# Kernel optimization log

Hardware: AMD Instinct MI355X
Metric: run time of the kernel (lower is better)

The kernel has to match this reference:

```python
import jax, jax.numpy as jnp
import numpy as np

B, L = 1024, 64          # sentences, tokens per sentence
V, E = 100000, 300       # vocab, embedding dim
RH, M, NC = 50, 50, 3    # rnn_hidden, mem_dim, num_class
N = B * L                # total tree nodes


def setup_inputs() -> dict:
    key = jax.random.key(0)
    ks = jax.random.split(key, 24)
    rn = lambda k, s, sc=0.05: jax.random.normal(k, s, dtype=jnp.float32) * sc
    # balanced binary dependency tree per sentence: parent(i) = (i-1)//2
    loc = np.arange(L)
    par_loc = np.where(loc == 0, -1, (loc - 1) // 2)
    parent = np.where(par_loc[None, :] < 0, -1,
                      par_loc[None, :] + np.arange(B)[:, None] * L).reshape(-1)
    depth = np.tile(np.floor(np.log2(loc + 1)).astype(np.int64), B)
    tm = np.zeros(L, np.float32); tm[1:4] = 1.0  # 3 aspect-target tokens/sentence
    return {
        "embed_ids": jax.random.randint(ks[0], (B, L), 0, V),
        "parent": jnp.asarray(parent),
        "depth": jnp.asarray(depth),
        "target_mask": jnp.asarray(np.tile(tm, B)),
        "num_levels": 7,
        "embed_table": rn(ks[1], (V, E), 1.0),
        "W_ih_f": rn(ks[2], (4 * RH, E)), "W_hh_f": rn(ks[3], (4 * RH, RH)),
        "b_f": rn(ks[4], (4 * RH,)),
        "W_ih_b": rn(ks[5], (4 * RH, E)), "W_hh_b": rn(ks[6], (4 * RH, RH)),
        "b_b": rn(ks[7], (4 * RH,)),
        "W_iou": rn(ks[8], (3 * M, 2 * RH)),
        "U_iou_w": rn(ks[9], (3 * M, M)), "U_iou_b": rn(ks[10], (3 * M,)),
        "b_iou": jnp.zeros((3 * M,), jnp.float32),
        "U_f_w": rn(ks[11], (M, M)), "U_f_b": rn(ks[12], (M,)),
        "H_w": rn(ks[13], (M, 2 * RH)), "H_b": rn(ks[14], (M,)),
        "C_w": rn(ks[15], (NC, M)), "C_b": rn(ks[16], (NC,)),
    }


def _lstm(x, W_ih, W_hh, b, reverse):
    # x: (B, L, E) -> (B, L, H); PyTorch gate order i, f, g, o
    xg = jnp.einsum('ble,ge->blg', x, W_ih) + b
    H = W_hh.shape[1]
    def step(carry, xt):
        h, c = carry
        g = xt + h @ W_hh.T
        i, f, gg, o = jnp.split(g, 4, axis=-1)
        c = jax.nn.sigmoid(f) * c + jax.nn.sigmoid(i) * jnp.tanh(gg)
        h = jax.nn.sigmoid(o) * jnp.tanh(c)
        return (h, c), h
    z = jnp.zeros((x.shape[0], H), x.dtype)
    _, hs = jax.lax.scan(step, (z, z), jnp.swapaxes(xg, 0, 1), reverse=reverse)
    return jnp.swapaxes(hs, 0, 1)


def reference(embed_ids, parent, depth, target_mask, num_levels, embed_table,
              W_ih_f, W_hh_f, b_f, W_ih_b, W_hh_b, b_b,
              W_iou, U_iou_w, U_iou_b, b_iou, U_f_w, U_f_b,
              H_w, H_b, C_w, C_b):
    # --- BiLSTM encoder (dropout = identity at inference) ---
    emb = embed_table[embed_ids]                       # (B,L,E) gather
    hf = _lstm(emb, W_ih_f, W_hh_f, b_f, False)
    hb = _lstm(emb, W_ih_b, W_hh_b, b_b, True)
    x = jnp.concatenate([hf, hb], -1).reshape(N, 2 * RH)
    # --- ChildSum TreeLSTM, topological (deepest level first) ---
    iou0 = x @ W_iou.T                                 # (N, 3M)
    h_init = x @ H_w.T + H_b                           # (N, M)
    parent_safe = jnp.where(parent >= 0, parent, N)    # roots -> dummy slot N
    counts = jnp.zeros(N + 1, jnp.int32).at[parent_safe].add(1)
    has_children = (counts[:N] > 0)[:, None]
    h_fin = h_init
    c_fin = jnp.zeros((N, M), jnp.float32)
    h_sum = jnp.zeros((N + 1, M), jnp.float32)         # sum of child h
    fc_sum = jnp.zeros((N + 1, M), jnp.float32)        # sum of f * child c
    for lvl in range(num_levels - 1, -1, -1):
        m = (depth == lvl)[:, None]
        # reduce: leaves never get U_iou bias (no mailbox in DGL)
        iou = iou0 + jnp.where(has_children, h_sum[:N] @ U_iou_w.T + U_iou_b, 0.0) + b_iou
        i, o, u = jnp.split(iou, 3, axis=-1)
        c_new = jax.nn.sigmoid(i) * jnp.tanh(u) + fc_sum[:N]
        h_new = h_init + jax.nn.sigmoid(o) * jnp.tanh(c_new)
        h_fin = jnp.where(m, h_new, h_fin)
        c_fin = jnp.where(m, c_new, c_fin)
        # scatter messages from this level's nodes to their parents
        f = jax.nn.sigmoid(h_new @ U_f_w.T + U_f_b)
        h_sum = h_sum.at[parent_safe].add(jnp.where(m, h_new, 0.0))
        fc_sum = fc_sum.at[parent_safe].add(jnp.where(m, f * c_new, 0.0))
    # --- masked mean pool over target tokens per sentence ---
    tm = target_mask.reshape(B, L)
    pooled = (h_fin.reshape(B, L, M) * tm[:, :, None]).sum(1) / tm.sum(1, keepdims=True)
    logits = pooled @ C_w.T + C_b
    return logits, pooled
```

## Files before the change

kernel.cpp:

```cpp
#include <hip/hip_runtime.h>


typedef __attribute__((ext_vector_type(8))) short bf16x8;
typedef __attribute__((ext_vector_type(4))) float f32x4;

__device__ __forceinline__ float fsig2(float x) {
    float e = __builtin_amdgcn_exp2f(-1.4426950408889634f * x);
    return __builtin_amdgcn_rcpf(1.0f + e);
}
__device__ __forceinline__ float ftanh2(float x) {
    float e = __builtin_amdgcn_exp2f(2.8853900817779268f * x);
    return 1.0f - 2.0f * __builtin_amdgcn_rcpf(1.0f + e);
}

__device__ __forceinline__ unsigned short rne_bf16(float f) {
    unsigned u = __builtin_bit_cast(unsigned, f);
    unsigned r = u + 0x7fffu + ((u >> 16) & 1u);
    return (unsigned short)(r >> 16);
}
__device__ __forceinline__ void split2(float f, unsigned short& h, unsigned short& l) {
    h = rne_bf16(f);
    float fh = __builtin_bit_cast(float, ((unsigned)h) << 16);
    float r = f - fh;
    l = rne_bf16(r);
}

__device__ __forceinline__ void async_lds16(const void* g, void* l) {
    __builtin_amdgcn_global_load_lds(
        (const __attribute__((address_space(1))) unsigned int*)g,
        (__attribute__((address_space(3))) unsigned int*)l, 16, 0, 0);
}

__device__ __forceinline__ bf16x8 pack8(const unsigned short* h) {
    bf16x8 v;
    #pragma unroll
    for (int e = 0; e < 8; ++e) v[e] = (short)h[e];
    return v;
}

__device__ __forceinline__ void conv_item(int q, const float* __restrict__ B1,
                                          const float* __restrict__ B2,
                                          int split, int K, int Rreal, int BN,
                                          unsigned short* __restrict__ out) {
    int n  = q % BN;
    int kq = (q / BN) & 3;
    int c  = q / (BN * 4);
    const float* row = (n < split) ? (B1 + (size_t)n * K) : (B2 + (size_t)(n - split) * K);
    unsigned short h[8], l[8];
    #pragma unroll
    for (int e = 0; e < 8; ++e) {
        int k = c * 32 + kq * 8 + e;
        float v = (n < Rreal && k < K) ? row[k] : 0.0f;
        split2(v, h[e], l[e]);
    }
    size_t hb = ((((size_t)c * 2 + 0) * 4 + kq) * BN + n) * 8;
    size_t lb = ((((size_t)c * 2 + 1) * 4 + kq) * BN + n) * 8;
    *(ushort4*)&out[hb]     = make_ushort4(h[0], h[1], h[2], h[3]);
    *(ushort4*)&out[hb + 4] = make_ushort4(h[4], h[5], h[6], h[7]);
    *(ushort4*)&out[lb]     = make_ushort4(l[0], l[1], l[2], l[3]);
    *(ushort4*)&out[lb + 4] = make_ushort4(l[4], l[5], l[6], l[7]);
}

constexpr int WHC_DIR = 2 * 2 * 4 * 208 * 8;

__global__ void conv_fused(const float* __restrict__ Wihf, const float* __restrict__ Wihb,
                           const float* __restrict__ Wiou, const float* __restrict__ Hw,
                           const float* __restrict__ Whhf, const float* __restrict__ Whhb,
                           unsigned short* __restrict__ B1c,
                           unsigned short* __restrict__ B3c,
                           unsigned short* __restrict__ Whc) {
    int q = blockIdx.x * 256 + threadIdx.x;
    if (q < 17920) {
        conv_item(q, Wihf, Wihb, 200, 300, 400, 448, B1c);
    } else if (q < 22016) {
        conv_item(q - 17920, Wiou, Hw, 150, 100, 200, 256, B3c);
    } else if (q < 23680) {
        conv_item(q - 22016, Whhf, Whhf, 200, 50, 200, 208, Whc);
    } else if (q < 25344) {
        conv_item(q - 23680, Whhb, Whhb, 200, 50, 200, 208, Whc + WHC_DIR);
    }
}

template<int BN, int KCH, int KREAL, int NCOLS, bool GATHER>
__global__ __launch_bounds__(256)
void gemm_split(const float* __restrict__ A, const int* __restrict__ ids,
                const unsigned short* __restrict__ Bc,
                const float* __restrict__ bias1, const float* __restrict__ bias2,
                int split, float* __restrict__ C) {
    constexpr int NTW = BN / 64;
    __shared__ __align__(16) unsigned short As[2 * 4 * 64 * 8];
    __shared__ __align__(16) unsigned short Bt[64 * BN];

    const int tid = threadIdx.x;
    const int m0 = blockIdx.x * 64;
    const int w = tid >> 6, lane = tid & 63;
    const int r16 = lane & 15, quad = lane >> 4;
    const int wn = w * (BN / 4);

    const int mA = tid & 63, kqA = tid >> 6;
    const float* arow = GATHER ? (A + (size_t)ids[m0 + mA] * KREAL)
                               : (A + (size_t)(m0 + mA) * KREAL);

    float ar[8];
    {
        int k0 = kqA * 8;
        if (k0 + 8 <= KREAL) {
            float4 p = *(const float4*)(arow + k0);
            float4 q = *(const float4*)(arow + k0 + 4);
            ar[0]=p.x; ar[1]=p.y; ar[2]=p.z; ar[3]=p.w;
            ar[4]=q.x; ar[5]=q.y; ar[6]=q.z; ar[7]=q.w;
        } else {
            #pragma unroll
            for (int e = 0; e < 8; ++e) ar[e] = (k0 + e < KREAL) ? arow[k0 + e] : 0.0f;
        }
    }

    f32x4 acc[4][NTW] = {};

    for (int c = 0; c < KCH; ++c) {
        __syncthreads();
        {
            const unsigned short* src = Bc + (size_t)c * 64 * BN + tid * 8;
            #pragma unroll
            for (int i = 0; i < BN / 32; ++i)
                async_lds16(src + (size_t)i * 2048, Bt + i * 2048 + tid * 8);
        }
        {
            unsigned short h[8], l[8];
            #pragma unroll
            for (int e = 0; e < 8; ++e) split2(ar[e], h[e], l[e]);
            *(bf16x8*)&As[((0 * 4 + kqA) * 64 + mA) * 8] = pack8(h);
            *(bf16x8*)&As[((1 * 4 + kqA) * 64 + mA) * 8] = pack8(l);
        }
        __syncthreads();
        if (c + 1 < KCH) {
            int k0 = (c + 1) * 32 + kqA * 8;
            if (k0 + 8 <= KREAL) {
                float4 p = *(const float4*)(arow + k0);
                float4 q = *(const float4*)(arow + k0 + 4);
                ar[0]=p.x; ar[1]=p.y; ar[2]=p.z; ar[3]=p.w;
                ar[4]=q.x; ar[5]=q.y; ar[6]=q.z; ar[7]=q.w;
            } else {
                #pragma unroll
                for (int e = 0; e < 8; ++e) ar[e] = (k0 + e < KREAL) ? arow[k0 + e] : 0.0f;
            }
        }
        bf16x8 af[2][4];
        #pragma unroll
        for (int i = 0; i < 4; ++i) {
            af[0][i] = *(const bf16x8*)&As[((0 * 4 + quad) * 64 + i * 16 + r16) * 8];
            af[1][i] = *(const bf16x8*)&As[((1 * 4 + quad) * 64 + i * 16 + r16) * 8];
        }
        #pragma unroll
        for (int t = 0; t < NTW; ++t) {
            bf16x8 bh = *(const bf16x8*)&Bt[((0 * 4 + quad) * BN + wn + t * 16 + r16) * 8];
            bf16x8 bl = *(const bf16x8*)&Bt[((1 * 4 + quad) * BN + wn + t * 16 + r16) * 8];
            #pragma unroll
            for (int i = 0; i < 4; ++i) {
                acc[i][t] = __builtin_amdgcn_mfma_f32_16x16x32_bf16(af[0][i], bh, acc[i][t], 0, 0, 0);
                acc[i][t] = __builtin_amdgcn_mfma_f32_16x16x32_bf16(af[1][i], bh, acc[i][t], 0, 0, 0);
                acc[i][t] = __builtin_amdgcn_mfma_f32_16x16x32_bf16(af[0][i], bl, acc[i][t], 0, 0, 0);
            }
        }
    }

    #pragma unroll
    for (int t = 0; t < NTW; ++t) {
        int ncol = wn + t * 16 + r16;
        if (ncol < NCOLS) {
            float bv = (ncol < split) ? bias1[ncol] : bias2[ncol - split];
            #pragma unroll
            for (int i = 0; i < 4; ++i)
                #pragma unroll
                for (int r = 0; r < 4; ++r) {
                    int mrow = m0 + i * 16 + quad * 4 + r;
                    C[(size_t)mrow * NCOLS + ncol] = acc[i][t][r] + bv;
                }
        }
    }
}

__global__ __launch_bounds__(256)
void lstm_mfma(const float* __restrict__ xg, const unsigned short* __restrict__ Whc,
               float* __restrict__ x) {
    const int bi = blockIdx.x;
    const int dir = bi & 1;
    const int b0 = (bi >> 1) * 8;
    const int tid = threadIdx.x;
    const int w = tid >> 6, lane = tid & 63;
    const int r16 = lane & 15, quad = lane >> 4;

    __shared__ __align__(16) unsigned short Ah[8 * 16 * 8];
    __shared__ __align__(16) unsigned short Al[8 * 16 * 8];
    __shared__ __align__(16) float G[208 * 20];
    __shared__ __align__(16) float Xs[3][8][268];

    const int n0 = (w == 0) ? 0 : (w == 1) ? 4 : (w == 2) ? 7 : 10;
    const int nc = (w == 0) ? 4 : 3;

    const unsigned short* Wd = Whc + (size_t)dir * WHC_DIR;
    bf16x8 bfr[4][2][2];
    #pragma unroll
    for (int t = 0; t < 4; ++t) {
        int col = (n0 + ((t < nc) ? t : 0)) * 16 + r16;
        #pragma unroll
        for (int c = 0; c < 2; ++c)
            #pragma unroll
            for (int h = 0; h < 2; ++h)
                bfr[t][c][h] = *(const bf16x8*)&Wd[((((size_t)c * 2 + h) * 4 + quad) * 208 + col) * 8];
    }

    for (int q = tid; q < 512; q += 256) {
        ((unsigned*)Ah)[q] = 0u;
        ((unsigned*)Al)[q] = 0u;
    }

    int ss[2], ms[2];
    bool act[2];
    #pragma unroll
    for (int j = 0; j < 2; ++j) {
        int q = w * 100 + lane + 64 * j;
        ss[j] = q & 7;
        ms[j] = q >> 3;
        act[j] = (lane + 64 * j) < 100;
    }
    float c_reg[2] = {0.0f, 0.0f};

    #pragma unroll
    for (int p = 0; p < 2; ++p) {
        int idx0 = dir ? (63 - p) : p;
        #pragma unroll
        for (int i = 0; i < 2; ++i) {
            int s = w * 2 + i;
            const float* src = xg + ((size_t)(b0 + s) * 64 + idx0) * 400 + dir * 200 + lane * 4;
            async_lds16(src, &Xs[p][s][lane * 4]);
        }
    }
    __syncthreads();

    for (int step = 0; step < 64; ++step) {
        const int buf = step % 3;
        const int idx = dir ? (63 - step) : step;
        {
            int stepn = step + 2; if (stepn > 63) stepn = 63;
            const int slot = (step + 2) % 3;
            const int idxn = dir ? (63 - stepn) : stepn;
            #pragma unroll
            for (int i = 0; i < 2; ++i) {
                int s = w * 2 + i;
                const float* src = xg + ((size_t)(b0 + s) * 64 + idxn) * 400 + dir * 200 + lane * 4;
                async_lds16(src, &Xs[slot][s][lane * 4]);
            }
            __builtin_amdgcn_sched_barrier(0);
        }
        bf16x8 ah[2], al[2];
        #pragma unroll
        for (int c = 0; c < 2; ++c) {
            ah[c] = *(const bf16x8*)&Ah[((c * 4 + quad) * 16 + r16) * 8];
            al[c] = *(const bf16x8*)&Al[((c * 4 + quad) * 16 + r16) * 8];
        }
        f32x4 acc[4] = {};
        #pragma unroll
        for (int t = 0; t < 4; ++t) {
            if (t < nc) {
                #pragma unroll
                for (int c = 0; c < 2; ++c) {
                    acc[t] = __builtin_amdgcn_mfma_f32_16x16x32_bf16(ah[c], bfr[t][c][0], acc[t], 0, 0, 0);
                    acc[t] = __builtin_amdgcn_mfma_f32_16x16x32_bf16(al[c], bfr[t][c][0], acc[t], 0, 0, 0);
                    acc[t] = __builtin_amdgcn_mfma_f32_16x16x32_bf16(ah[c], bfr[t][c][1], acc[t], 0, 0, 0);
                }
            }
        }
        #pragma unroll
        for (int t = 0; t < 4; ++t) {
            if (t < nc) {
                int col = (n0 + t) * 16 + r16;
                *(f32x4*)&G[col * 20 + quad * 4] = acc[t];
            }
        }
        asm volatile("s_waitcnt lgkmcnt(0) vmcnt(8)" ::: "memory");
        __builtin_amdgcn_sched_barrier(0);
        __builtin_amdgcn_s_barrier();
        __builtin_amdgcn_sched_barrier(0);
        #pragma unroll
        for (int j = 0; j < 2; ++j) {
            if (act[j]) {
                int s = ss[j], m = ms[j];
                float gi = G[m * 20 + s]         + Xs[buf][s][m];
                float gf = G[(m + 50) * 20 + s]  + Xs[buf][s][m + 50];
                float gg = G[(m + 100) * 20 + s] + Xs[buf][s][m + 100];
                float go = G[(m + 150) * 20 + s] + Xs[buf][s][m + 150];
                c_reg[j] = fsig2(gf) * c_reg[j] + fsig2(gi) * ftanh2(gg);
                float h = fsig2(go) * ftanh2(c_reg[j]);
                unsigned short hh, hl;
                split2(h, hh, hl);
                Ah[(m >> 3) * 128 + s * 8 + (m & 7)] = hh;
                Al[(m >> 3) * 128 + s * 8 + (m & 7)] = hl;
                x[((size_t)(b0 + s) * 64 + idx) * 100 + dir * 50 + m] = h;
            }
        }
        asm volatile("s_waitcnt lgkmcnt(0)" ::: "memory");
        __builtin_amdgcn_sched_barrier(0);
        __builtin_amdgcn_s_barrier();
        __builtin_amdgcn_sched_barrier(0);
    }
}

__global__ __launch_bounds__(256)
void tree_kernel(const float* __restrict__ C2,
                 const float* __restrict__ Uw, const float* __restrict__ Ub,
                 const float* __restrict__ Fw, const float* __restrict__ Fb,
                 const float* __restrict__ tmask,
                 const float* __restrict__ Cw, const float* __restrict__ Cb,
                 float* __restrict__ out) {
    const int b = blockIdx.x;
    const int tid = threadIdx.x;

    __shared__ __align__(16) float Us[150][52];
    __shared__ __align__(16) float h_sum[32][52];
    __shared__ __align__(16) float fc_sum[32][52];
    __shared__ __align__(16) float hcur[32][52];
    __shared__ float mcur[32][50];
    __shared__ float pool[52];
    __shared__ float tms[64];

    for (int q = tid; q < 7500; q += 256) Us[q / 50][q % 50] = Uw[q];
    for (int q = tid; q < 32 * 52; q += 256) {
        h_sum[q / 52][q % 52] = 0.0f;
        fc_sum[q / 52][q % 52] = 0.0f;
    }
    if (tid < 64) tms[tid] = tmask[(size_t)b * 64 + tid];
    if (tid < 52) pool[tid] = 0.0f;
    __syncthreads();

    const float* c2b = C2 + (size_t)b * 64 * 200;

    for (int lvl = 6; lvl >= 0; --lvl) {
        const int lo = (1 << lvl) - 1;
        const int hi = min((1 << (lvl + 1)) - 2, 63);
        const int A = hi - lo + 1;
        const int chn = max(0, min(hi, 31) - lo + 1);

        for (int q = tid; q < A * 50; q += 256) {
            int a = q / 50, m = q - a * 50;
            int loc = lo + a;
            const float* base = c2b + (size_t)loc * 200;
            bool ch = (a < chn);
            float mi = 0.0f, mo = 0.0f, mu = 0.0f, fcv = 0.0f;
            if (ch) {
                float4 H[12];
                #pragma unroll
                for (int j = 0; j < 12; ++j) H[j] = *(const float4*)&h_sum[loc][j * 4];
                float h48 = h_sum[loc][48], h49 = h_sum[loc][49];
                const float* u0 = &Us[m][0];
                const float* u1 = &Us[50 + m][0];
                const float* u2 = &Us[100 + m][0];
                float i0=0,i1=0,i2=0,i3=0, o0=0,o1=0,o2=0,o3=0, g0=0,g1=0,g2=0,g3=0;
                #pragma unroll
                for (int j = 0; j < 12; ++j) {
                    float4 a4 = *(const float4*)&u0[j * 4];
                    float4 b4 = *(const float4*)&u1[j * 4];
                    float4 c4 = *(const float4*)&u2[j * 4];
                    i0 += a4.x*H[j].x; i1 += a4.y*H[j].y; i2 += a4.z*H[j].z; i3 += a4.w*H[j].w;
                    o0 += b4.x*H[j].x; o1 += b4.y*H[j].y; o2 += b4.z*H[j].z; o3 += b4.w*H[j].w;
                    g0 += c4.x*H[j].x; g1 += c4.y*H[j].y; g2 += c4.z*H[j].z; g3 += c4.w*H[j].w;
                }
                mi = Ub[m]       + (i0 + i1) + (i2 + i3) + u0[48]*h48 + u0[49]*h49;
                mo = Ub[50 + m]  + (o0 + o1) + (o2 + o3) + u1[48]*h48 + u1[49]*h49;
                mu = Ub[100 + m] + (g0 + g1) + (g2 + g3) + u2[48]*h48 + u2[49]*h49;
                fcv = fc_sum[loc][m];
            }
            float ig = base[m] + mi;
            float og = base[50 + m] + mo;
            float ug = base[100 + m] + mu;
            float cn = fsig2(ig) * ftanh2(ug) + fcv;
            float hn = base[150 + m] + fsig2(og) * ftanh2(cn);
            hcur[a][m] = hn;
            mcur[a][m] = cn;
            float tv = tms[loc];
            if (tv != 0.0f) atomicAdd(&pool[m], tv * hn);
        }
        __syncthreads();

        if (lvl > 0) {
            for (int q = tid; q < A * 50; q += 256) {
                int a = q / 50, m = q - a * 50;
                int loc = lo + a;
                const float* frow = Fw + m * 50;
                const float* hc = &hcur[a][0];
                float a0 = 0, a1 = 0, a2 = 0, a3 = 0;
                #pragma unroll
                for (int j = 0; j < 12; ++j) {
                    float4 f4 = *(const float4*)&frow[j * 4];
                    float4 h4 = *(const float4*)&hc[j * 4];
                    a0 += f4.x*h4.x; a1 += f4.y*h4.y; a2 += f4.z*h4.z; a3 += f4.w*h4.w;
                }
                float acc = Fb[m] + (a0 + a1) + (a2 + a3)
                          + frow[48]*hc[48] + frow[49]*hc[49];
                float fm = fsig2(acc) * mcur[a][m];
                int p = (loc - 1) >> 1;
                atomicAdd(&h_sum[p][m], hcur[a][m]);
                atomicAdd(&fc_sum[p][m], fm);
            }
        }
        __syncthreads();
    }

    if (tid < 50) {
        float ws = 0.0f;
        #pragma unroll
        for (int l = 0; l < 64; ++l) ws += tms[l];
        float p = pool[tid] / ws;
        pool[tid] = p;
        out[3072 + (size_t)b * 50 + tid] = p;
    }
    __syncthreads();
    if (tid < 3) {
        float acc = Cb[tid];
        #pragma unroll
        for (int m = 0; m < 50; ++m) acc += Cw[tid * 50 + m] * pool[m];
        out[(size_t)b * 3 + tid] = acc;
    }
}

extern "C" void kernel_launch(void* const* d_in, const int* in_sizes, int n_in,
                              void* d_out, int out_size, void* d_ws, size_t ws_size,
                              hipStream_t stream) {
    (void)in_sizes; (void)n_in; (void)out_size; (void)ws_size;
    const int*   ids   = (const int*)d_in[0];
    const float* tmask = (const float*)d_in[3];
    const float* table = (const float*)d_in[5];
    const float* Wihf  = (const float*)d_in[6];
    const float* Whhf  = (const float*)d_in[7];
    const float* bf    = (const float*)d_in[8];
    const float* Wihb  = (const float*)d_in[9];
    const float* Whhb  = (const float*)d_in[10];
    const float* bb    = (const float*)d_in[11];
    const float* Wiou  = (const float*)d_in[12];
    const float* Uiouw = (const float*)d_in[13];
    const float* Uioub = (const float*)d_in[14];
    const float* biou  = (const float*)d_in[15];
    const float* Ufw   = (const float*)d_in[16];
    const float* Ufb   = (const float*)d_in[17];
    const float* Hw    = (const float*)d_in[18];
    const float* Hb    = (const float*)d_in[19];
    const float* Cw    = (const float*)d_in[20];
    const float* Cb    = (const float*)d_in[21];
    float* out = (float*)d_out;

    float* wsf = (float*)d_ws;
    float* xg = wsf;
    float* x  = wsf + (size_t)65536 * 400;
    float* C2 = wsf;
    unsigned short* B1c = (unsigned short*)(wsf + 32768000);
    unsigned short* B3c = (unsigned short*)(wsf + 32911360);
    unsigned short* Whc = (unsigned short*)(wsf + 32944128);

    conv_fused<<<99, 256, 0, stream>>>(Wihf, Wihb, Wiou, Hw, Whhf, Whhb,
                                       B1c, B3c, Whc);
    gemm_split<448, 10, 300, 400, true><<<1024, 256, 0, stream>>>(
        table, ids, B1c, bf, bb, 200, xg);
    lstm_mfma<<<256, 256, 0, stream>>>(xg, Whc, x);
    gemm_split<256, 4, 100, 200, false><<<1024, 256, 0, stream>>>(
        x, nullptr, B3c, biou, Hb, 150, C2);
    tree_kernel<<<1024, 256, 0, stream>>>(
        C2, Uiouw, Uioub, Ufw, Ufb, tmask, Cw, Cb, out);
}
```

Measured before the change: 437.6 us.

## Process one sentence per wavefront in tree kernel, removing block barriers and atomics

The tree kernel now assigns each sentence to one 64-lane wavefront, with four sentences per block and 256 blocks instead of 1024. Nodes are walked sequentially within each wave, so the per-level __syncthreads and LDS atomics are replaced by plain wave-local LDS updates. The next node's C2 row is prefetched into registers, and U_f is cached in LDS. This trades node-level parallelism for no inter-wave synchronisation, at the cost of a long serial chain of 63 node steps per wave and relying on implicit wave-synchronous LDS ordering.

```diff
diff --git a/kernel.cpp b/kernel.cpp
--- a/kernel.cpp
+++ b/kernel.cpp
@@ -313,113 +313,117 @@
                  const float* __restrict__ tmask,
                  const float* __restrict__ Cw, const float* __restrict__ Cb,
                  float* __restrict__ out) {
-    const int b = blockIdx.x;
     const int tid = threadIdx.x;
+    const int w = tid >> 6, lane = tid & 63;
+    const int s = blockIdx.x * 4 + w;
 
     __shared__ __align__(16) float Us[150][52];
-    __shared__ __align__(16) float h_sum[32][52];
-    __shared__ __align__(16) float fc_sum[32][52];
-    __shared__ __align__(16) float hcur[32][52];
-    __shared__ float mcur[32][50];
-    __shared__ float pool[52];
-    __shared__ float tms[64];
+    __shared__ __align__(16) float Fs[50][52];
+    __shared__ __align__(16) float HS[4][32][52];
+    __shared__ __align__(16) float FC[4][32][52];
+    __shared__ __align__(16) float HV[4][64];
+    __shared__ __align__(16) float TMS[4][64];
 
     for (int q = tid; q < 7500; q += 256) Us[q / 50][q % 50] = Uw[q];
-    for (int q = tid; q < 32 * 52; q += 256) {
-        h_sum[q / 52][q % 52] = 0.0f;
-        fc_sum[q / 52][q % 52] = 0.0f;
-    }
-    if (tid < 64) tms[tid] = tmask[(size_t)b * 64 + tid];
-    if (tid < 52) pool[tid] = 0.0f;
+    for (int q = tid; q < 2500; q += 256) Fs[q / 50][q % 50] = Fw[q];
+    for (int q = tid; q < 4 * 32 * 52; q += 256) {
+        int ww = q / (32 * 52), r = q - ww * (32 * 52);
+        HS[ww][r / 52][r % 52] = 0.0f;
+        FC[ww][r / 52][r % 52] = 0.0f;
+    }
+    TMS[w][lane] = tmask[(size_t)s * 64 + lane];
     __syncthreads();
 
-    const float* c2b = C2 + (size_t)b * 64 * 200;
-
-    for (int lvl = 6; lvl >= 0; --lvl) {
-        const int lo = (1 << lvl) - 1;
-        const int hi = min((1 << (lvl + 1)) - 2, 63);
-        const int A = hi - lo + 1;
-        const int chn = max(0, min(hi, 31) - lo + 1);
-
-        for (int q = tid; q < A * 50; q += 256) {
-            int a = q / 50, m = q - a * 50;
-            int loc = lo + a;
-            const float* base = c2b + (size_t)loc * 200;
-            bool ch = (a < chn);
+    const bool act = lane < 50;
+    const int m = act ? lane : 49;
+    const float ub0 = Ub[m], ub1 = Ub[50 + m], ub2 = Ub[100 + m];
+    const float fb = Fb[m];
+    const float* c2s = C2 + (size_t)s * 64 * 200;
+
+    float pr = 0.0f;
+    float pc0, pc1, pc2, pc3;
+    {
+        const float* nb = c2s + 63 * 200;
+        pc0 = nb[m]; pc1 = nb[50 + m]; pc2 = nb[100 + m]; pc3 = nb[150 + m];
+    }
+
+    for (int l = 6; l >= 0; --l) {
+        const int lo = (1 << l) - 1;
+        const int hi = min((1 << (l + 1)) - 2, 63);
+        for (int loc = lo; loc <= hi; ++loc) {
+            const int nxt = (loc < hi) ? (loc + 1) : ((l > 0) ? ((1 << (l - 1)) - 1) : loc);
+            float nc0, nc1, nc2, nc3;
+            {
+                const float* nb = c2s + (size_t)nxt * 200;
+                nc0 = nb[m]; nc1 = nb[50 + m]; nc2 = nb[100 + m]; nc3 = nb[150 + m];
+            }
+            const bool hasch = (loc <= 31);
             float mi = 0.0f, mo = 0.0f, mu = 0.0f, fcv = 0.0f;
-            if (ch) {
-                float4 H[12];
-                #pragma unroll
-                for (int j = 0; j < 12; ++j) H[j] = *(const float4*)&h_sum[loc][j * 4];
-                float h48 = h_sum[loc][48], h49 = h_sum[loc][49];
+            if (hasch) {
+                const float* hs = &HS[w][loc][0];
                 const float* u0 = &Us[m][0];
                 const float* u1 = &Us[50 + m][0];
                 const float* u2 = &Us[100 + m][0];
                 float i0=0,i1=0,i2=0,i3=0, o0=0,o1=0,o2=0,o3=0, g0=0,g1=0,g2=0,g3=0;
                 #pragma unroll
                 for (int j = 0; j < 12; ++j) {
+                    float4 h4 = *(const float4*)&hs[j * 4];
                     float4 a4 = *(const float4*)&u0[j * 4];
                     float4 b4 = *(const float4*)&u1[j * 4];
                     float4 c4 = *(const float4*)&u2[j * 4];
-                    i0 += a4.x*H[j].x; i1 += a4.y*H[j].y; i2 += a4.z*H[j].z; i3 += a4.w*H[j].w;
-                    o0 += b4.x*H[j].x; o1 += b4.y*H[j].y; o2 += b4.z*H[j].z; o3 += b4.w*H[j].w;
-                    g0 += c4.x*H[j].x; g1 += c4.y*H[j].y; g2 += c4.z*H[j].z; g3 += c4.w*H[j].w;
+                    i0 += a4.x*h4.x; i1 += a4.y*h4.y; i2 += a4.z*h4.z; i3 += a4.w*h4.w;
+                    o0 += b4.x*h4.x; o1 += b4.y*h4.y; o2 += b4.z*h4.z; o3 += b4.w*h4.w;
+                    g0 += c4.x*h4.x; g1 += c4.y*h4.y; g2 += c4.z*h4.z; g3 += c4.w*h4.w;
                 }
-                mi = Ub[m]       + (i0 + i1) + (i2 + i3) + u0[48]*h48 + u0[49]*h49;
-                mo = Ub[50 + m]  + (o0 + o1) + (o2 + o3) + u1[48]*h48 + u1[49]*h49;
-                mu = Ub[100 + m] + (g0 + g1) + (g2 + g3) + u2[48]*h48 + u2[49]*h49;
-                fcv = fc_sum[loc][m];
-            }
-            float ig = base[m] + mi;
-            float og = base[50 + m] + mo;
-            float ug = base[100 + m] + mu;
+                float h48 = hs[48], h49 = hs[49];
+                mi = ub0 + (i0 + i1) + (i2 + i3) + u0[48]*h48 + u0[49]*h49;
+                mo = ub1 + (o0 + o1) + (o2 + o3) + u1[48]*h48 + u1[49]*h49;
+                mu = ub2 + (g0 + g1) + (g2 + g3) + u2[48]*h48 + u2[49]*h49;
+                fcv = FC[w][loc][m];
+            }
+            float ig = pc0 + mi, og = pc1 + mo, ug = pc2 + mu;
             float cn = fsig2(ig) * ftanh2(ug) + fcv;
-            float hn = base[150 + m] + fsig2(og) * ftanh2(cn);
-            hcur[a][m] = hn;
-            mcur[a][m] = cn;
-            float tv = tms[loc];
-            if (tv != 0.0f) atomicAdd(&pool[m], tv * hn);
-        }
-        __syncthreads();
-
-        if (lvl > 0) {
-            for (int q = tid; q < A * 50; q += 256) {
-                int a = q / 50, m = q - a * 50;
-                int loc = lo + a;
-                const float* frow = Fw + m * 50;
-                const float* hc = &hcur[a][0];
+            float hn = pc3 + fsig2(og) * ftanh2(cn);
+            pr += TMS[w][loc] * hn;
+            if (act) HV[w][lane] = hn;
+            {
+                const float* hv = &HV[w][0];
+                const float* f0 = &Fs[m][0];
                 float a0 = 0, a1 = 0, a2 = 0, a3 = 0;
                 #pragma unroll
                 for (int j = 0; j < 12; ++j) {
-                    float4 f4 = *(const float4*)&frow[j * 4];
-                    float4 h4 = *(const float4*)&hc[j * 4];
+                    float4 h4 = *(const float4*)&hv[j * 4];
+                    float4 f4 = *(const float4*)&f0[j * 4];
                     a0 += f4.x*h4.x; a1 += f4.y*h4.y; a2 += f4.z*h4.z; a3 += f4.w*h4.w;
                 }
-                float acc = Fb[m] + (a0 + a1) + (a2 + a3)
-                          + frow[48]*hc[48] + frow[49]*hc[49];
-                float fm = fsig2(acc) * mcur[a][m];
-                int p = (loc - 1) >> 1;
-                atomicAdd(&h_sum[p][m], hcur[a][m]);
-                atomicAdd(&fc_sum[p][m], fm);
-            }
-        }
-        __syncthreads();
-    }
-
-    if (tid < 50) {
-        float ws = 0.0f;
-        #pragma unroll
-        for (int l = 0; l < 64; ++l) ws += tms[l];
-        float p = pool[tid] / ws;
-        pool[tid] = p;
-        out[3072 + (size_t)b * 50 + tid] = p;
-    }
-    __syncthreads();
-    if (tid < 3) {
-        float acc = Cb[tid];
-        #pragma unroll
-        for (int m = 0; m < 50; ++m) acc += Cw[tid * 50 + m] * pool[m];
-        out[(size_t)b * 3 + tid] = acc;
+                float facc = fb + (a0 + a1) + (a2 + a3) + f0[48]*hv[48] + f0[49]*hv[49];
+                if (act && loc > 0) {
+                    int p = (loc - 1) >> 1;
+                    float fm = fsig2(facc) * cn;
+                    HS[w][p][lane] += hn;
+                    FC[w][p][lane] += fm;
+                }
+            }
+            pc0 = nc0; pc1 = nc1; pc2 = nc2; pc3 = nc3;
+        }
+    }
+
+    float ws = 0.0f;
+    #pragma unroll
+    for (int j = 0; j < 16; ++j) {
+        float4 t4 = *(const float4*)&TMS[w][j * 4];
+        ws += (t4.x + t4.y) + (t4.z + t4.w);
+    }
+    float p = pr / ws;
+    if (act) {
+        out[3072 + (size_t)s * 50 + lane] = p;
+        HV[w][lane] = p;
+    }
+    if (lane < 3) {
+        float acc = Cb[lane];
+        const float* crow = Cw + lane * 50;
+        for (int k = 0; k < 50; ++k) acc += crow[k] * HV[w][k];
+        out[(size_t)s * 3 + lane] = acc;
     }
 }
 
@@ -463,6 +467,6 @@
     lstm_mfma<<<256, 256, 0, stream>>>(xg, Whc, x);
     gemm_split<256, 4, 100, 200, false><<<1024, 256, 0, stream>>>(
         x, nullptr, B3c, biou, Hb, 150, C2);
-    tree_kernel<<<1024, 256, 0, stream>>>(
+    tree_kernel<<<256, 256, 0, stream>>>(
         C2, Uiouw, Uioub, Ufw, Ufb, tmask, Cw, Cb, out);
 }
```

Result: faster. 418.6 us (-4.3%).
